# Performance work log

Measured on AMD Instinct MI355X. Metric: run time of the kernel, lower is better.

Reference implementation:

```python
import jax, jax.numpy as jnp
import numpy as np

K = 7      # kernel_size
PAD = 3    # padding ('same' with stride 1)
G = 16     # groups


def _unfold(x):
    """torch nn.Unfold equivalent, stride=1, dilation=1.
    Returns [B, C, K*K, H, W] with kernel positions ordered (kh, kw),
    matching torch's (c, kh, kw) channel-major layout after reshape."""
    B, C, H, W = x.shape
    xp = jnp.pad(x, ((0, 0), (0, 0), (PAD, PAD), (PAD, PAD)))
    patches = jnp.stack(
        [xp[:, :, i:i + H, j:j + W] for i in range(K) for j in range(K)],
        axis=2,
    )
    return patches


def setup_inputs() -> dict:
    key = jax.random.key(0)
    k1, k2, k3 = jax.random.split(key, 3)
    B, C, H, W = 4, 256, 64, 64
    x = jax.random.normal(k1, (B, C, H, W), dtype=jnp.float32)
    # 1x1 conv producing kernel_prod*groups = 49*16 = 784 channels (with bias)
    w_kernel = jax.random.normal(k2, (G * K * K, C), dtype=jnp.float32) * 0.05
    b_kernel = jax.random.normal(k3, (G * K * K,), dtype=jnp.float32) * 0.05
    return {"x": x, "w_kernel": w_kernel, "b_kernel": b_kernel}


def reference(x, w_kernel, b_kernel):
    B, C, H, W = x.shape
    Cg = C // G
    # unfolded input: [B, G, C//G, K*K, H, W]
    patches = _unfold(x).reshape(B, G, Cg, K * K, H, W)
    # dynamic per-pixel kernel: AvgPool(k=1) is identity at stride 1,
    # then 1x1 conv with bias -> [B, G*K*K, H, W]
    kern = jnp.einsum('bchw,kc->bkhw', x, w_kernel) + b_kernel[None, :, None, None]
    kern = kern.reshape(B, G, 1, K * K, H, W)
    # multiply and sum-reduce over kernel positions, flatten groups
    out = (patches * kern).sum(axis=3).reshape(B, C, H, W)
    return out
```

## Files before the change

### kernel.cpp

```cpp
#include <hip/hip_runtime.h>


#define B_   4
#define C_   256
#define G_   16
#define KK_  49
#define KS_  7
#define PD_  3

#define XP8_BYTES (B_*32*4096*8*2)
#define WBF_OFF   XP8_BYTES

#define SKW   28
#define HC_   70
#define HPOS  (10*HC_)

typedef __attribute__((ext_vector_type(8))) short bf16x8;
typedef __attribute__((ext_vector_type(4))) float f32x4;
typedef unsigned short ushort_t;

__device__ inline unsigned f2bf(float f) {
    unsigned u = __float_as_uint(f);
    u += 0x7FFF + ((u >> 16) & 1);
    return u >> 16;
}

__global__ __launch_bounds__(256)
void cvt_xp8(const float* __restrict__ x, const float* __restrict__ wk,
             ushort_t* __restrict__ xp8, unsigned* __restrict__ wbf) {
    const int t = threadIdx.x;
    if (blockIdx.x == 64) {
        const int slice = blockIdx.z * 4 + blockIdx.y;
        const float2* wk2 = (const float2*)wk;
        const int base = slice * 6272;
        for (int k = t; k < 6272; k += 256) {
            float2 v = wk2[base + k];
            wbf[base + k] = f2bf(v.x) | (f2bf(v.y) << 16);
        }
        return;
    }
    __shared__ float tile[64][65];
    const int p0 = blockIdx.x * 64;
    const int c0 = blockIdx.y * 64;
    const int b  = blockIdx.z;
    const int px_r = t & 63;
    #pragma unroll
    for (int i = 0; i < 16; ++i) {
        int ch = (t >> 6) + i * 4;
        tile[ch][px_r] = x[((size_t)(b * C_ + c0 + ch) << 12) + p0 + px_r];
    }
    __syncthreads();
    const int px = t & 63;
    const int ob = t >> 6;
    #pragma unroll
    for (int jj = 0; jj < 2; ++jj) {
        const int j = ob + jj * 4;
        unsigned u[4];
        #pragma unroll
        for (int k2 = 0; k2 < 4; ++k2) {
            float a0 = tile[j * 8 + 2 * k2][px];
            float a1 = tile[j * 8 + 2 * k2 + 1][px];
            u[k2] = f2bf(a0) | (f2bf(a1) << 16);
        }
        ushort_t* dst = xp8 + (((size_t)((b << 5) + (c0 >> 3) + j) << 12) + p0 + px) * 8;
        *(uint4*)dst = make_uint4(u[0], u[1], u[2], u[3]);
    }
}

__device__ inline uint4 stage_ld(const ushort_t* __restrict__ xp8,
                                 int b, int oct, int gy0, int e) {
    const int row = e / HC_;
    const int col = e - row * HC_;
    const int sy = gy0 + row - PD_;
    const int sx = col - PD_;
    if (sy >= 0 && sy < 64 && sx >= 0 && sx < 64)
        return *(const uint4*)(xp8 + (((size_t)((b << 5) + oct) << 12) + sy * 64 + sx) * 8);
    return make_uint4(0u, 0u, 0u, 0u);
}

__global__ __launch_bounds__(256, 4)
void inv_fused(const ushort_t* __restrict__ xp8,
               const ushort_t* __restrict__ wbf,
               const float* __restrict__ bk,
               float* __restrict__ out) {
    __shared__ unsigned kern2[256 * SKW];
    __shared__ unsigned halo4[HPOS * 4];

    const int bid  = blockIdx.x;
    const int g    = bid >> 6;
    const int b    = (bid >> 4) & 3;
    const int tile = bid & 15;
    const int gy0  = tile * 4;
    const int p0   = tile * 256;

    const int tid  = threadIdx.x;
    const int wv   = tid >> 6;
    const int ln15 = tid & 15;
    const int quad = (tid & 63) >> 4;

    f32x4 acc[16];
    #pragma unroll
    for (int i = 0; i < 16; ++i) acc[i] = (f32x4){0.f, 0.f, 0.f, 0.f};

    const ushort_t* ap[4];
    #pragma unroll
    for (int mt = 0; mt < 4; ++mt) {
        int r = mt * 16 + ln15; if (r > KK_ - 1) r = KK_ - 1;
        ap[mt] = wbf + (size_t)(g * KK_ + r) * C_ + quad * 8;
    }
    const ushort_t* bp = xp8 + (((size_t)((b << 5) + quad) << 12) + p0 + wv * 64 + ln15) * 8;

    bf16x8 af[2][4], bf[2][4];
    #pragma unroll
    for (int mt = 0; mt < 4; ++mt) af[0][mt] = *(const bf16x8*)(ap[mt]);
    #pragma unroll
    for (int nt = 0; nt < 4; ++nt) bf[0][nt] = *(const bf16x8*)(bp + nt * 128);

    #pragma unroll
    for (int k = 0; k < 8; ++k) {
        const int cur = k & 1, nxt = cur ^ 1;
        if (k < 7) {
            const int cc = (k + 1) * 32;
            #pragma unroll
            for (int mt = 0; mt < 4; ++mt)
                af[nxt][mt] = *(const bf16x8*)(ap[mt] + cc);
            #pragma unroll
            for (int nt = 0; nt < 4; ++nt)
                bf[nxt][nt] = *(const bf16x8*)(bp + ((size_t)cc << 12) + nt * 128);
        }
        #pragma unroll
        for (int mt = 0; mt < 4; ++mt) {
            #pragma unroll
            for (int nt = 0; nt < 4; ++nt) {
                acc[mt * 4 + nt] = __builtin_amdgcn_mfma_f32_16x16x32_bf16(
                    af[cur][mt], bf[cur][nt], acc[mt * 4 + nt], 0, 0, 0);
            }
        }
    }

    for (int e = tid; e < HPOS; e += 256)
        *(uint4*)&halo4[e * 4] = stage_ld(xp8, b, 2 * g, gy0, e);

    #pragma unroll
    for (int mt = 0; mt < 3; ++mt) {
        const int m0 = mt * 16 + quad * 4;
        const float b0 = bk[g * KK_ + m0],     b1 = bk[g * KK_ + m0 + 1];
        const float b2 = bk[g * KK_ + m0 + 2], b3 = bk[g * KK_ + m0 + 3];
        #pragma unroll
        for (int nt = 0; nt < 4; ++nt) {
            const int p = wv * 64 + nt * 16 + ln15;
            uint2 d;
            d.x = f2bf(acc[mt * 4 + nt][0] + b0) | (f2bf(acc[mt * 4 + nt][1] + b1) << 16);
            d.y = f2bf(acc[mt * 4 + nt][2] + b2) | (f2bf(acc[mt * 4 + nt][3] + b3) << 16);
            *(uint2*)&kern2[p * SKW + mt * 8 + quad * 2] = d;
        }
    }
    if (quad == 0) {
        const float b48 = bk[g * KK_ + 48];
        #pragma unroll
        for (int nt = 0; nt < 4; ++nt) {
            const int p = wv * 64 + nt * 16 + ln15;
            kern2[p * SKW + 24] = f2bf(acc[12 + nt][0] + b48);
        }
    }
    __syncthreads();

    float kv[KK_];
    {
        const uint4* kr = (const uint4*)&kern2[tid * SKW];
        unsigned kd[28];
        #pragma unroll
        for (int q = 0; q < 7; ++q) {
            uint4 h = kr[q];
            kd[4*q] = h.x; kd[4*q+1] = h.y; kd[4*q+2] = h.z; kd[4*q+3] = h.w;
        }
        #pragma unroll
        for (int k = 0; k < KK_; ++k) {
            unsigned d = kd[k >> 1];
            kv[k] = __uint_as_float((k & 1) ? (d & 0xffff0000u) : (d << 16));
        }
    }

    uint4 pf0 = stage_ld(xp8, b, 2 * g + 1, gy0, tid);
    uint4 pf1 = stage_ld(xp8, b, 2 * g + 1, gy0, tid + 256);
    uint4 pf2 = (tid < HPOS - 512) ? stage_ld(xp8, b, 2 * g + 1, gy0, tid + 512)
                                   : make_uint4(0u, 0u, 0u, 0u);

    const int py = tid >> 6, px = tid & 63;

    #pragma unroll 1
    for (int hb = 0; hb < 2; ++hb) {
        if (hb) {
            __syncthreads();
            *(uint4*)&halo4[tid * 4] = pf0;
            *(uint4*)&halo4[(tid + 256) * 4] = pf1;
            if (tid < HPOS - 512) *(uint4*)&halo4[(tid + 512) * 4] = pf2;
            __syncthreads();
        }
        float a[8];
        #pragma unroll
        for (int q = 0; q < 8; ++q) a[q] = 0.f;
        #pragma unroll
        for (int kh = 0; kh < KS_; ++kh) {
            const uint4* hr = (const uint4*)&halo4[((py + kh) * HC_ + px) * 4];
            #pragma unroll
            for (int kw = 0; kw < KS_; ++kw) {
                uint4 hv = hr[kw];
                float kk = kv[kh * KS_ + kw];
                a[0] = fmaf(__uint_as_float(hv.x << 16),          kk, a[0]);
                a[1] = fmaf(__uint_as_float(hv.x & 0xffff0000u),  kk, a[1]);
                a[2] = fmaf(__uint_as_float(hv.y << 16),          kk, a[2]);
                a[3] = fmaf(__uint_as_float(hv.y & 0xffff0000u),  kk, a[3]);
                a[4] = fmaf(__uint_as_float(hv.z << 16),          kk, a[4]);
                a[5] = fmaf(__uint_as_float(hv.z & 0xffff0000u),  kk, a[5]);
                a[6] = fmaf(__uint_as_float(hv.w << 16),          kk, a[6]);
                a[7] = fmaf(__uint_as_float(hv.w & 0xffff0000u),  kk, a[7]);
            }
        }
        const size_t o = ((size_t)(b * C_ + g * 16 + hb * 8) << 12) + p0 + tid;
        #pragma unroll
        for (int q = 0; q < 8; ++q)
            out[o + ((size_t)q << 12)] = a[q];
    }
}

extern "C" void kernel_launch(void* const* d_in, const int* in_sizes, int n_in,
                              void* d_out, int out_size, void* d_ws, size_t ws_size,
                              hipStream_t stream) {
    const float* x  = (const float*)d_in[0];
    const float* wk = (const float*)d_in[1];
    const float* bk = (const float*)d_in[2];
    float* o = (float*)d_out;

    ushort_t* xp8 = (ushort_t*)d_ws;
    unsigned* wbf = (unsigned*)((char*)d_ws + WBF_OFF);

    cvt_xp8<<<dim3(65, 4, B_), dim3(256), 0, stream>>>(x, wk, xp8, wbf);
    inv_fused<<<dim3(1024), dim3(256), 0, stream>>>(
        xp8, (const ushort_t*)wbf, bk, o);
}
```

Before: 106.4 us.

## Split fused dynamic-kernel GEMM and involution apply into separate kernels

```diff
diff --git a/kernel.cpp b/kernel.cpp
--- a/kernel.cpp
+++ b/kernel.cpp
@@ -5,13 +5,15 @@
 #define C_   256
 #define G_   16
 #define KK_  49
+#define M_   784
 #define KS_  7
 #define PD_  3
 
-#define XP8_BYTES (B_*32*4096*8*2)
-#define WBF_OFF   XP8_BYTES
-
-#define SKW   28
+#define KERN_BYTES (B_*M_*4096*2)
+#define XP8_BYTES  (B_*32*4096*8*2)
+#define XP8_OFF    KERN_BYTES
+#define WBF_OFF    (KERN_BYTES + XP8_BYTES)
+
 #define HC_   70
 #define HPOS  (10*HC_)
 
@@ -23,6 +25,9 @@
     unsigned u = __float_as_uint(f);
     u += 0x7FFF + ((u >> 16) & 1);
     return u >> 16;
+}
+__device__ inline float bf2f(unsigned short s) {
+    return __uint_as_float(((unsigned)s) << 16);
 }
 
 __global__ __launch_bounds__(256)
@@ -67,6 +72,86 @@
     }
 }
 
+__global__ __launch_bounds__(256, 4)
+void kern_gemm(const ushort_t* __restrict__ xp8,
+               const ushort_t* __restrict__ wbf,
+               const float* __restrict__ bk,
+               ushort_t* __restrict__ kern) {
+    const int bid  = blockIdx.x;
+    const int g    = bid >> 6;
+    const int b    = (bid >> 4) & 3;
+    const int tile = bid & 15;
+    const int p0   = tile * 256;
+
+    const int tid  = threadIdx.x;
+    const int wv   = tid >> 6;
+    const int ln15 = tid & 15;
+    const int quad = (tid & 63) >> 4;
+
+    f32x4 acc[16];
+    #pragma unroll
+    for (int i = 0; i < 16; ++i) acc[i] = (f32x4){0.f, 0.f, 0.f, 0.f};
+
+    const ushort_t* ap[4];
+    #pragma unroll
+    for (int mt = 0; mt < 4; ++mt) {
+        int r = mt * 16 + ln15; if (r > KK_ - 1) r = KK_ - 1;
+        ap[mt] = wbf + (size_t)(g * KK_ + r) * C_ + quad * 8;
+    }
+    const ushort_t* bp = xp8 + (((size_t)((b << 5) + quad) << 12) + p0 + wv * 64 + ln15) * 8;
+
+    bf16x8 af[2][4], bf[2][4];
+    #pragma unroll
+    for (int mt = 0; mt < 4; ++mt) af[0][mt] = *(const bf16x8*)(ap[mt]);
+    #pragma unroll
+    for (int nt = 0; nt < 4; ++nt) bf[0][nt] = *(const bf16x8*)(bp + nt * 128);
+
+    #pragma unroll
+    for (int k = 0; k < 8; ++k) {
+        const int cur = k & 1, nxt = cur ^ 1;
+        if (k < 7) {
+            const int cc = (k + 1) * 32;
+            #pragma unroll
+            for (int mt = 0; mt < 4; ++mt)
+                af[nxt][mt] = *(const bf16x8*)(ap[mt] + cc);
+            #pragma unroll
+            for (int nt = 0; nt < 4; ++nt)
+                bf[nxt][nt] = *(const bf16x8*)(bp + ((size_t)cc << 12) + nt * 128);
+        }
+        #pragma unroll
+        for (int mt = 0; mt < 4; ++mt) {
+            #pragma unroll
+            for (int nt = 0; nt < 4; ++nt) {
+                acc[mt * 4 + nt] = __builtin_amdgcn_mfma_f32_16x16x32_bf16(
+                    af[cur][mt], bf[cur][nt], acc[mt * 4 + nt], 0, 0, 0);
+            }
+        }
+    }
+
+    const size_t kb0 = ((size_t)(b * M_ + g * KK_) << 12) + p0 + wv * 64 + ln15;
+    #pragma unroll
+    for (int mt = 0; mt < 3; ++mt) {
+        #pragma unroll
+        for (int r = 0; r < 4; ++r) {
+            const int m = mt * 16 + quad * 4 + r;
+            const float bias = bk[g * KK_ + m];
+            #pragma unroll
+            for (int nt = 0; nt < 4; ++nt) {
+                kern[kb0 + ((size_t)m << 12) + nt * 16] =
+                    (ushort_t)f2bf(acc[mt * 4 + nt][r] + bias);
+            }
+        }
+    }
+    if (quad == 0) {
+        const float b48 = bk[g * KK_ + 48];
+        #pragma unroll
+        for (int nt = 0; nt < 4; ++nt) {
+            kern[kb0 + ((size_t)48 << 12) + nt * 16] =
+                (ushort_t)f2bf(acc[12 + nt][0] + b48);
+        }
+    }
+}
+
 __device__ inline uint4 stage_ld(const ushort_t* __restrict__ xp8,
                                  int b, int oct, int gy0, int e) {
     const int row = e / HC_;
@@ -78,12 +163,10 @@
     return make_uint4(0u, 0u, 0u, 0u);
 }
 
-__global__ __launch_bounds__(256, 4)
-void inv_fused(const ushort_t* __restrict__ xp8,
-               const ushort_t* __restrict__ wbf,
-               const float* __restrict__ bk,
+__global__ __launch_bounds__(256, 5)
+void inv_apply(const ushort_t* __restrict__ xp8,
+               const ushort_t* __restrict__ kern,
                float* __restrict__ out) {
-    __shared__ unsigned kern2[256 * SKW];
     __shared__ unsigned halo4[HPOS * 4];
 
     const int bid  = blockIdx.x;
@@ -93,93 +176,18 @@
     const int gy0  = tile * 4;
     const int p0   = tile * 256;
 
-    const int tid  = threadIdx.x;
-    const int wv   = tid >> 6;
-    const int ln15 = tid & 15;
-    const int quad = (tid & 63) >> 4;
-
-    f32x4 acc[16];
-    #pragma unroll
-    for (int i = 0; i < 16; ++i) acc[i] = (f32x4){0.f, 0.f, 0.f, 0.f};
-
-    const ushort_t* ap[4];
-    #pragma unroll
-    for (int mt = 0; mt < 4; ++mt) {
-        int r = mt * 16 + ln15; if (r > KK_ - 1) r = KK_ - 1;
-        ap[mt] = wbf + (size_t)(g * KK_ + r) * C_ + quad * 8;
-    }
-    const ushort_t* bp = xp8 + (((size_t)((b << 5) + quad) << 12) + p0 + wv * 64 + ln15) * 8;
-
-    bf16x8 af[2][4], bf[2][4];
-    #pragma unroll
-    for (int mt = 0; mt < 4; ++mt) af[0][mt] = *(const bf16x8*)(ap[mt]);
-    #pragma unroll
-    for (int nt = 0; nt < 4; ++nt) bf[0][nt] = *(const bf16x8*)(bp + nt * 128);
-
-    #pragma unroll
-    for (int k = 0; k < 8; ++k) {
-        const int cur = k & 1, nxt = cur ^ 1;
-        if (k < 7) {
-            const int cc = (k + 1) * 32;
-            #pragma unroll
-            for (int mt = 0; mt < 4; ++mt)
-                af[nxt][mt] = *(const bf16x8*)(ap[mt] + cc);
-            #pragma unroll
-            for (int nt = 0; nt < 4; ++nt)
-                bf[nxt][nt] = *(const bf16x8*)(bp + ((size_t)cc << 12) + nt * 128);
-        }
-        #pragma unroll
-        for (int mt = 0; mt < 4; ++mt) {
-            #pragma unroll
-            for (int nt = 0; nt < 4; ++nt) {
-                acc[mt * 4 + nt] = __builtin_amdgcn_mfma_f32_16x16x32_bf16(
-                    af[cur][mt], bf[cur][nt], acc[mt * 4 + nt], 0, 0, 0);
-            }
-        }
+    const int tid = threadIdx.x;
+
+    float kv[KK_];
+    {
+        const ushort_t* kb = kern + ((size_t)(b * M_ + g * KK_) << 12) + p0 + tid;
+        #pragma unroll
+        for (int j = 0; j < KK_; ++j) kv[j] = bf2f(kb[(size_t)j << 12]);
     }
 
     for (int e = tid; e < HPOS; e += 256)
         *(uint4*)&halo4[e * 4] = stage_ld(xp8, b, 2 * g, gy0, e);
-
-    #pragma unroll
-    for (int mt = 0; mt < 3; ++mt) {
-        const int m0 = mt * 16 + quad * 4;
-        const float b0 = bk[g * KK_ + m0],     b1 = bk[g * KK_ + m0 + 1];
-        const float b2 = bk[g * KK_ + m0 + 2], b3 = bk[g * KK_ + m0 + 3];
-        #pragma unroll
-        for (int nt = 0; nt < 4; ++nt) {
-            const int p = wv * 64 + nt * 16 + ln15;
-            uint2 d;
-            d.x = f2bf(acc[mt * 4 + nt][0] + b0) | (f2bf(acc[mt * 4 + nt][1] + b1) << 16);
-            d.y = f2bf(acc[mt * 4 + nt][2] + b2) | (f2bf(acc[mt * 4 + nt][3] + b3) << 16);
-            *(uint2*)&kern2[p * SKW + mt * 8 + quad * 2] = d;
-        }
-    }
-    if (quad == 0) {
-        const float b48 = bk[g * KK_ + 48];
-        #pragma unroll
-        for (int nt = 0; nt < 4; ++nt) {
-            const int p = wv * 64 + nt * 16 + ln15;
-            kern2[p * SKW + 24] = f2bf(acc[12 + nt][0] + b48);
-        }
-    }
     __syncthreads();
-
-    float kv[KK_];
-    {
-        const uint4* kr = (const uint4*)&kern2[tid * SKW];
-        unsigned kd[28];
-        #pragma unroll
-        for (int q = 0; q < 7; ++q) {
-            uint4 h = kr[q];
-            kd[4*q] = h.x; kd[4*q+1] = h.y; kd[4*q+2] = h.z; kd[4*q+3] = h.w;
-        }
-        #pragma unroll
-        for (int k = 0; k < KK_; ++k) {
-            unsigned d = kd[k >> 1];
-            kv[k] = __uint_as_float((k & 1) ? (d & 0xffff0000u) : (d << 16));
-        }
-    }
 
     uint4 pf0 = stage_ld(xp8, b, 2 * g + 1, gy0, tid);
     uint4 pf1 = stage_ld(xp8, b, 2 * g + 1, gy0, tid + 256);
@@ -232,10 +240,13 @@
     const float* bk = (const float*)d_in[2];
     float* o = (float*)d_out;
 
-    ushort_t* xp8 = (ushort_t*)d_ws;
-    unsigned* wbf = (unsigned*)((char*)d_ws + WBF_OFF);
+    ushort_t* kern_ws = (ushort_t*)d_ws;
+    ushort_t* xp8     = (ushort_t*)((char*)d_ws + XP8_OFF);
+    unsigned* wbf     = (unsigned*)((char*)d_ws + WBF_OFF);
 
     cvt_xp8<<<dim3(65, 4, B_), dim3(256), 0, stream>>>(x, wk, xp8, wbf);
-    inv_fused<<<dim3(1024), dim3(256), 0, stream>>>(
-        xp8, (const ushort_t*)wbf, bk, o);
-}
+    kern_gemm<<<dim3(1024), dim3(256), 0, stream>>>(
+        xp8, (const ushort_t*)wbf, bk, kern_ws);
+    inv_apply<<<dim3(1024), dim3(256), 0, stream>>>(
+        xp8, kern_ws, o);
+}
```

Result: slower. 114.1 us (+7.3%).
